# Kernel tuning notes

Measured on AMD Instinct MI355X. Metric: run time of the kernel, lower is better.

The kernel has to match this reference:

```python
import jax, jax.numpy as jnp
import numpy as np

N_NODES = 40000
N_EDGES = 640000
IN_DIM = 7
HID = 128
N_LAYERS = 5


def setup_inputs() -> dict:
    key = jax.random.key(0)
    ks = jax.random.split(key, 12)
    x = jax.random.normal(ks[0], (N_NODES, IN_DIM), dtype=jnp.float32)
    edge_index = jax.random.randint(ks[1], (2, N_EDGES), 0, N_NODES, dtype=jnp.int64)
    # shift distances away from 0 so 1/d^2 weights stay finite across 5 layers
    dist = jax.random.uniform(ks[2], (N_EDGES,), dtype=jnp.float32) + 0.5
    s_enc = 1.0 / np.sqrt(IN_DIM)
    s_hid = 1.0 / np.sqrt(HID)
    enc_W = jax.random.normal(ks[3], (HID, IN_DIM), dtype=jnp.float32) * s_enc
    enc_b = jax.random.normal(ks[4], (HID,), dtype=jnp.float32) * 0.01
    conv_W = jax.random.normal(ks[5], (N_LAYERS, HID, HID), dtype=jnp.float32) * s_hid * 0.2
    conv_b = jax.random.normal(ks[6], (N_LAYERS, HID), dtype=jnp.float32) * 0.01
    cluster_W = jax.random.normal(ks[7], (3, HID), dtype=jnp.float32) * s_hid
    cluster_b = jax.random.normal(ks[8], (3,), dtype=jnp.float32) * 0.01
    energy_W = jax.random.normal(ks[9], (1, HID), dtype=jnp.float32) * s_hid
    energy_b = jax.random.normal(ks[10], (1,), dtype=jnp.float32) * 0.01
    return {"x": x, "edge_index": edge_index, "dist": dist,
            "enc_W": enc_W, "enc_b": enc_b,
            "conv_W": conv_W, "conv_b": conv_b,
            "cluster_W": cluster_W, "cluster_b": cluster_b,
            "energy_W": energy_W, "energy_b": energy_b}


def reference(x, edge_index, dist, enc_W, enc_b, conv_W, conv_b,
              cluster_W, cluster_b, energy_W, energy_b):
    n = x.shape[0]
    src = edge_index[0]  # x_j: source nodes (PyG source_to_target flow)
    dst = edge_index[1]  # aggregation target
    w = 1.0 / jnp.square(dist + 1e-6)  # [E]
    h = x @ enc_W.T + enc_b  # [N, H]
    for l in range(conv_W.shape[0]):
        # gather -> linear -> inverse-square weight -> scatter-add
        msg = (h[src] @ conv_W[l].T + conv_b[l]) * w[:, None]  # [E, H]
        h = jax.nn.relu(jax.ops.segment_sum(msg, dst, num_segments=n))
    cluster_probs = jax.nn.softmax(h @ cluster_W.T + cluster_b, axis=-1)  # [N, 3]
    energy = h.mean(axis=0, keepdims=True) @ energy_W.T + energy_b  # [1, 1]
    stable = energy < -1.0
    return cluster_probs, energy, stable
```

## Files before the change

kernel.cpp:

```cpp
#include <hip/hip_runtime.h>
#include <hip/hip_fp16.h>

#define NN 40000
#define NE 640000
#define HID 128
#define NL 5
#define NBLK 157

typedef __attribute__((ext_vector_type(8))) short bf16x8;
typedef __attribute__((ext_vector_type(4))) float f32x4;

static __device__ __forceinline__ unsigned short f32_to_bf16_rne(float f) {
  unsigned int u = __float_as_uint(f);
  unsigned int lsb = (u >> 16) & 1u;
  u += 0x7fffu + lsb;
  return (unsigned short)(u >> 16);
}
static __device__ __forceinline__ float bf16_to_f32(unsigned short s) {
  return __uint_as_float(((unsigned int)s) << 16);
}

__global__ void encoder_wconv_kernel(const float* __restrict__ x, const float* __restrict__ encW,
                                     const float* __restrict__ encb, __half* __restrict__ h,
                                     const float* __restrict__ convW,
                                     unsigned short* __restrict__ whi,
                                     unsigned short* __restrict__ wlo) {
  int b = blockIdx.x;
  if (b < 20000) {
    int gid = b * 256 + threadIdx.x;
    int n = gid >> 7, k = gid & 127;
    const float* xp = x + n * 7;
    const float* wp = encW + k * 7;
    float acc = encb[k];
#pragma unroll
    for (int i = 0; i < 7; ++i) acc += xp[i] * wp[i];
    h[gid] = __float2half(acc);
  } else {
    int i = (b - 20000) * 256 + threadIdx.x;
    if (i < NL * HID * HID) {
      float w = convW[i];
      unsigned short hi = f32_to_bf16_rne(w);
      unsigned short lo = f32_to_bf16_rne(w - bf16_to_f32(hi));
      whi[i] = hi;
      wlo[i] = lo;
    }
  }
}

__global__ void hist_kernel(const int* __restrict__ dst, int* __restrict__ cnt,
                            int* __restrict__ rank) {
  int e = blockIdx.x * blockDim.x + threadIdx.x;
  if (e < NE) rank[e] = atomicAdd(&cnt[dst[e]], 1);
}

__global__ void partial_kernel(const int* __restrict__ cnt, int* __restrict__ blocksum) {
  __shared__ int red[4];
  int t = threadIdx.x;
  int idx = blockIdx.x * 256 + t;
  int v = idx < NN ? cnt[idx] : 0;
#pragma unroll
  for (int off = 32; off > 0; off >>= 1) v += __shfl_xor(v, off, 64);
  if ((t & 63) == 0) red[t >> 6] = v;
  __syncthreads();
  if (t == 0) blocksum[blockIdx.x] = red[0] + red[1] + red[2] + red[3];
}

__global__ void scan_small_kernel(const int* __restrict__ blocksum, int* __restrict__ blockoff,
                                  int* __restrict__ row_ptr) {
  __shared__ int sh[256];
  int t = threadIdx.x;
  int v = t < NBLK ? blocksum[t] : 0;
  sh[t] = v;
  __syncthreads();
  for (int off = 1; off < 256; off <<= 1) {
    int u = (t >= off) ? sh[t - off] : 0;
    __syncthreads();
    sh[t] += u;
    __syncthreads();
  }
  if (t < NBLK) blockoff[t] = sh[t] - v;
  if (t == 255) row_ptr[NN] = sh[255];
}

__global__ void rowptr_kernel(const int* __restrict__ cnt, const int* __restrict__ blockoff,
                              int* __restrict__ row_ptr) {
  __shared__ int sh[256];
  int t = threadIdx.x;
  int idx = blockIdx.x * 256 + t;
  int v = idx < NN ? cnt[idx] : 0;
  sh[t] = v;
  __syncthreads();
  for (int off = 1; off < 256; off <<= 1) {
    int u = (t >= off) ? sh[t - off] : 0;
    __syncthreads();
    sh[t] += u;
    __syncthreads();
  }
  if (idx < NN) row_ptr[idx] = blockoff[blockIdx.x] + sh[t] - v;
}

__global__ void scatter_kernel(const int* __restrict__ src, const int* __restrict__ dst,
                               const float* __restrict__ dist,
                               const int* __restrict__ row_ptr, const int* __restrict__ rank,
                               int2* __restrict__ csr_ew) {
  int e = blockIdx.x * blockDim.x + threadIdx.x;
  if (e >= NE) return;
  int pos = row_ptr[dst[e]] + rank[e];
  float dd = dist[e] + 1e-6f;
  float w = 1.0f / (dd * dd);
  csr_ew[pos] = make_int2(src[e], (int)__float_as_uint(w));
}

__global__ void wsum_kernel(const int* __restrict__ row_ptr, const int2* __restrict__ csr_ew,
                            float* __restrict__ wsum) {
  int n = blockIdx.x * blockDim.x + threadIdx.x;
  if (n >= NN) return;
  int s = row_ptr[n], e = row_ptr[n + 1];
  float acc = 0.f;
  for (int i = s; i < e; ++i) acc += __uint_as_float((unsigned)csr_ew[i].y);
  wsum[n] = acc;
}

__global__ void aggregate_kernel(const __half* __restrict__ h, const int* __restrict__ row_ptr,
                                 const int2* __restrict__ csr_ew,
                                 unsigned short* __restrict__ aggh,
                                 unsigned short* __restrict__ aggl) {
  int wid = (blockIdx.x * blockDim.x + threadIdx.x) >> 6;
  int lane = threadIdx.x & 63;
  if (wid >= NN) return;
  int s = __builtin_amdgcn_readfirstlane(row_ptr[wid]);
  int e = __builtin_amdgcn_readfirstlane(row_ptr[wid + 1]);
  const __half* hp = h + lane * 2;
  float ax = 0.f, ay = 0.f;
  int i = s;
  for (; i + 16 <= e; i += 16) {
    unsigned hv[16];
    float wv[16];
#pragma unroll
    for (int u = 0; u < 16; ++u) {
      int2 p = csr_ew[i + u];
      wv[u] = __uint_as_float((unsigned)p.y);
      hv[u] = *reinterpret_cast<const unsigned*>(hp + p.x * HID);
    }
#pragma unroll
    for (int u = 0; u < 16; ++u) {
      float2 f = __half22float2(*reinterpret_cast<__half2*>(&hv[u]));
      ax += wv[u] * f.x;
      ay += wv[u] * f.y;
    }
  }
  for (; i < e; ++i) {
    int2 p = csr_ew[i];
    float w = __uint_as_float((unsigned)p.y);
    float2 f = __half22float2(*reinterpret_cast<const __half2*>(hp + p.x * HID));
    ax += w * f.x;
    ay += w * f.y;
  }
  unsigned short hx = f32_to_bf16_rne(ax);
  unsigned short lx = f32_to_bf16_rne(ax - bf16_to_f32(hx));
  unsigned short hy = f32_to_bf16_rne(ay);
  unsigned short ly = f32_to_bf16_rne(ay - bf16_to_f32(hy));
  ushort2 hv2 = {hx, hy}, lv2 = {lx, ly};
  *reinterpret_cast<ushort2*>(aggh + wid * HID + lane * 2) = hv2;
  *reinterpret_cast<ushort2*>(aggl + wid * HID + lane * 2) = lv2;
}

__global__ void __launch_bounds__(256) mfma_linear_kernel(
    const unsigned short* __restrict__ aggh, const unsigned short* __restrict__ aggl,
    const unsigned short* __restrict__ whi, const unsigned short* __restrict__ wlo,
    const float* __restrict__ wsum, const float* __restrict__ b, __half* __restrict__ h) {
  int wave = threadIdx.x >> 6;
  int lane = threadIdx.x & 63;
  int node0 = blockIdx.x * 64 + wave * 16;
  int mrow = lane & 15;
  int kc = (lane >> 4) * 8;

  const unsigned short* pah = aggh + (node0 + mrow) * HID;
  const unsigned short* pal = aggl + (node0 + mrow) * HID;

  f32x4 acc[8];
#pragma unroll
  for (int t = 0; t < 8; ++t) acc[t] = (f32x4){0.f, 0.f, 0.f, 0.f};

#pragma unroll
  for (int s = 0; s < 4; ++s) {
    int joff = s * 32 + kc;
    bf16x8 ah = *reinterpret_cast<const bf16x8*>(pah + joff);
    bf16x8 al = *reinterpret_cast<const bf16x8*>(pal + joff);
#pragma unroll
    for (int t = 0; t < 8; ++t) {
      bf16x8 bh = *reinterpret_cast<const bf16x8*>(whi + (t * 16 + mrow) * HID + joff);
      bf16x8 bl = *reinterpret_cast<const bf16x8*>(wlo + (t * 16 + mrow) * HID + joff);
      acc[t] = __builtin_amdgcn_mfma_f32_16x16x32_bf16(ah, bh, acc[t], 0, 0, 0);
      acc[t] = __builtin_amdgcn_mfma_f32_16x16x32_bf16(ah, bl, acc[t], 0, 0, 0);
      acc[t] = __builtin_amdgcn_mfma_f32_16x16x32_bf16(al, bh, acc[t], 0, 0, 0);
    }
  }

  int nodeBase = node0 + (lane >> 4) * 4;
  float ws4[4];
#pragma unroll
  for (int r = 0; r < 4; ++r) ws4[r] = wsum[nodeBase + r];
#pragma unroll
  for (int t = 0; t < 8; ++t) {
    int kout = t * 16 + mrow;
    float bk = b[kout];
#pragma unroll
    for (int r = 0; r < 4; ++r) {
      float v = acc[t][r] + bk * ws4[r];
      h[(nodeBase + r) * HID + kout] = __float2half(fmaxf(v, 0.f));
    }
  }
}

__global__ void cluster_kernel(const __half* __restrict__ h, const float* __restrict__ cW,
                               const float* __restrict__ cb, float* __restrict__ out) {
  int wid = (blockIdx.x * blockDim.x + threadIdx.x) >> 6;
  int lane = threadIdx.x & 63;
  if (wid >= NN) return;
  float h0 = __half2float(h[wid * HID + lane]);
  float h1 = __half2float(h[wid * HID + 64 + lane]);
  float logit[3];
#pragma unroll
  for (int c = 0; c < 3; ++c) {
    float p = h0 * cW[c * HID + lane] + h1 * cW[c * HID + 64 + lane];
#pragma unroll
    for (int off = 32; off > 0; off >>= 1) p += __shfl_xor(p, off, 64);
    logit[c] = p + cb[c];
  }
  if (lane == 0) {
    float m = fmaxf(logit[0], fmaxf(logit[1], logit[2]));
    float e0 = expf(logit[0] - m), e1 = expf(logit[1] - m), e2 = expf(logit[2] - m);
    float inv = 1.0f / (e0 + e1 + e2);
    out[wid * 3 + 0] = e0 * inv;
    out[wid * 3 + 1] = e1 * inv;
    out[wid * 3 + 2] = e2 * inv;
  }
}

__global__ void colsum_part_kernel(const __half* __restrict__ h, float* __restrict__ partial) {
  int t = threadIdx.x;
  int col = t & 127;
  int lane_id = blockIdx.x * 2 + (t >> 7);
  float acc = 0.f;
  for (int r = lane_id; r < NN; r += 2048) acc += __half2float(h[r * HID + col]);
  partial[lane_id * HID + col] = acc;
}

__global__ void energy_final_kernel(const float* __restrict__ partial,
                                    const float* __restrict__ eW, const float* __restrict__ eb,
                                    float* __restrict__ out) {
  __shared__ float sh[8][HID];
  __shared__ float red[2];
  int t = threadIdx.x;
  int col = t & 127;
  int slot = t >> 7;
  float acc = 0.f;
  for (int i = 0; i < 256; ++i) acc += partial[(slot + 8 * i) * HID + col];
  sh[slot][col] = acc;
  __syncthreads();
  if (t < 128) {
    float s = 0.f;
#pragma unroll
    for (int j = 0; j < 8; ++j) s += sh[j][t];
    float v = s * (1.0f / NN) * eW[t];
#pragma unroll
    for (int off = 32; off > 0; off >>= 1) v += __shfl_xor(v, off, 64);
    if ((t & 63) == 0) red[t >> 6] = v;
  }
  __syncthreads();
  if (t == 0) {
    float e = red[0] + red[1] + eb[0];
    out[NN * 3] = e;
    out[NN * 3 + 1] = (e < -1.0f) ? 1.0f : 0.0f;
  }
}

extern "C" void kernel_launch(void* const* d_in, const int* in_sizes, int n_in,
                              void* d_out, int out_size, void* d_ws, size_t ws_size,
                              hipStream_t stream) {
  const float* x    = (const float*)d_in[0];
  const int*   ei   = (const int*)d_in[1];
  const float* dist = (const float*)d_in[2];
  const float* encW = (const float*)d_in[3];
  const float* encb = (const float*)d_in[4];
  const float* convW = (const float*)d_in[5];
  const float* convb = (const float*)d_in[6];
  const float* cW   = (const float*)d_in[7];
  const float* cb   = (const float*)d_in[8];
  const float* eW   = (const float*)d_in[9];
  const float* eb   = (const float*)d_in[10];
  float* out = (float*)d_out;

  char* ws = (char*)d_ws;
  __half*         h       = (__half*)        (ws + 0);
  unsigned short* aggh    = (unsigned short*)(ws + 10240000);
  unsigned short* aggl    = (unsigned short*)(ws + 20480000);
  int2*           csr_ew  = (int2*)          (ws + 30720000);
  int*            row_ptr = (int*)           (ws + 35840000);
  int*            cnt     = (int*)           (ws + 36000064);
  float*          wsum    = (float*)         (ws + 36160064);
  unsigned short* whi5    = (unsigned short*)(ws + 36320064);
  unsigned short* wlo5    = (unsigned short*)(ws + 36483904);
  int*            rank    = (int*)           (ws + 36647744);
  if (ws_size < (size_t)39207744) return;

  int*   blocksum = (int*)aggh;
  int*   blockoff = (int*)aggh + 512;
  float* partial  = (float*)aggh;

  const int* srcI = ei;
  const int* dstI = ei + NE;

  hipMemsetAsync(cnt, 0, 160000, stream);

  encoder_wconv_kernel<<<20320, 256, 0, stream>>>(x, encW, encb, h, convW, whi5, wlo5);

  hist_kernel<<<(NE + 255) / 256, 256, 0, stream>>>(dstI, cnt, rank);
  partial_kernel<<<NBLK, 256, 0, stream>>>(cnt, blocksum);
  scan_small_kernel<<<1, 256, 0, stream>>>(blocksum, blockoff, row_ptr);
  rowptr_kernel<<<NBLK, 256, 0, stream>>>(cnt, blockoff, row_ptr);
  scatter_kernel<<<(NE + 255) / 256, 256, 0, stream>>>(srcI, dstI, dist, row_ptr, rank, csr_ew);
  wsum_kernel<<<(NN + 255) / 256, 256, 0, stream>>>(row_ptr, csr_ew, wsum);

  for (int l = 0; l < NL; ++l) {
    aggregate_kernel<<<(NN * 64 + 255) / 256, 256, 0, stream>>>(h, row_ptr, csr_ew, aggh, aggl);
    mfma_linear_kernel<<<NN / 64, 256, 0, stream>>>(aggh, aggl,
                                                    whi5 + (size_t)l * HID * HID,
                                                    wlo5 + (size_t)l * HID * HID,
                                                    wsum, convb + (size_t)l * HID, h);
  }

  cluster_kernel<<<(NN * 64 + 255) / 256, 256, 0, stream>>>(h, cW, cb, out);
  colsum_part_kernel<<<1024, 256, 0, stream>>>(h, partial);
  energy_final_kernel<<<1, 1024, 0, stream>>>(partial, eW, eb, out);
}
```

Measured before the change: 410.1 us.

## Fuse neighbor aggregation into MFMA linear kernel via LDS staging

```diff
diff --git a/kernel.cpp b/kernel.cpp
--- a/kernel.cpp
+++ b/kernel.cpp
@@ -6,6 +6,7 @@
 #define HID 128
 #define NL 5
 #define NBLK 157
+#define LSTRIDE 136
 
 typedef __attribute__((ext_vector_type(8))) short bf16x8;
 typedef __attribute__((ext_vector_type(4))) float f32x4;
@@ -121,63 +122,58 @@
   wsum[n] = acc;
 }
 
-__global__ void aggregate_kernel(const __half* __restrict__ h, const int* __restrict__ row_ptr,
-                                 const int2* __restrict__ csr_ew,
-                                 unsigned short* __restrict__ aggh,
-                                 unsigned short* __restrict__ aggl) {
-  int wid = (blockIdx.x * blockDim.x + threadIdx.x) >> 6;
-  int lane = threadIdx.x & 63;
-  if (wid >= NN) return;
-  int s = __builtin_amdgcn_readfirstlane(row_ptr[wid]);
-  int e = __builtin_amdgcn_readfirstlane(row_ptr[wid + 1]);
-  const __half* hp = h + lane * 2;
-  float ax = 0.f, ay = 0.f;
-  int i = s;
-  for (; i + 16 <= e; i += 16) {
-    unsigned hv[16];
-    float wv[16];
-#pragma unroll
-    for (int u = 0; u < 16; ++u) {
-      int2 p = csr_ew[i + u];
-      wv[u] = __uint_as_float((unsigned)p.y);
-      hv[u] = *reinterpret_cast<const unsigned*>(hp + p.x * HID);
-    }
-#pragma unroll
-    for (int u = 0; u < 16; ++u) {
-      float2 f = __half22float2(*reinterpret_cast<__half2*>(&hv[u]));
-      ax += wv[u] * f.x;
-      ay += wv[u] * f.y;
-    }
-  }
-  for (; i < e; ++i) {
-    int2 p = csr_ew[i];
-    float w = __uint_as_float((unsigned)p.y);
-    float2 f = __half22float2(*reinterpret_cast<const __half2*>(hp + p.x * HID));
-    ax += w * f.x;
-    ay += w * f.y;
-  }
-  unsigned short hx = f32_to_bf16_rne(ax);
-  unsigned short lx = f32_to_bf16_rne(ax - bf16_to_f32(hx));
-  unsigned short hy = f32_to_bf16_rne(ay);
-  unsigned short ly = f32_to_bf16_rne(ay - bf16_to_f32(hy));
-  ushort2 hv2 = {hx, hy}, lv2 = {lx, ly};
-  *reinterpret_cast<ushort2*>(aggh + wid * HID + lane * 2) = hv2;
-  *reinterpret_cast<ushort2*>(aggl + wid * HID + lane * 2) = lv2;
-}
-
-__global__ void __launch_bounds__(256) mfma_linear_kernel(
-    const unsigned short* __restrict__ aggh, const unsigned short* __restrict__ aggl,
+__global__ void __launch_bounds__(256) fused_layer_kernel(
+    const __half* __restrict__ hin, const int* __restrict__ row_ptr,
+    const int2* __restrict__ csr_ew,
     const unsigned short* __restrict__ whi, const unsigned short* __restrict__ wlo,
-    const float* __restrict__ wsum, const float* __restrict__ b, __half* __restrict__ h) {
+    const float* __restrict__ wsum, const float* __restrict__ b,
+    __half* __restrict__ hout) {
+  __shared__ __align__(16) unsigned short sAh[4][16][LSTRIDE];
+  __shared__ __align__(16) unsigned short sAl[4][16][LSTRIDE];
   int wave = threadIdx.x >> 6;
   int lane = threadIdx.x & 63;
   int node0 = blockIdx.x * 64 + wave * 16;
+
+  const __half* hp = hin + lane * 2;
+  for (int t = 0; t < 16; ++t) {
+    int node = node0 + t;
+    int s = __builtin_amdgcn_readfirstlane(row_ptr[node]);
+    int e = __builtin_amdgcn_readfirstlane(row_ptr[node + 1]);
+    float ax = 0.f, ay = 0.f;
+    int i = s;
+    for (; i + 16 <= e; i += 16) {
+      unsigned hv[16];
+      float wv[16];
+#pragma unroll
+      for (int u = 0; u < 16; ++u) {
+        int2 p = csr_ew[i + u];
+        wv[u] = __uint_as_float((unsigned)p.y);
+        hv[u] = *reinterpret_cast<const unsigned*>(hp + p.x * HID);
+      }
+#pragma unroll
+      for (int u = 0; u < 16; ++u) {
+        float2 f = __half22float2(*reinterpret_cast<__half2*>(&hv[u]));
+        ax += wv[u] * f.x;
+        ay += wv[u] * f.y;
+      }
+    }
+    for (; i < e; ++i) {
+      int2 p = csr_ew[i];
+      float w = __uint_as_float((unsigned)p.y);
+      float2 f = __half22float2(*reinterpret_cast<const __half2*>(hp + p.x * HID));
+      ax += w * f.x;
+      ay += w * f.y;
+    }
+    unsigned short hx = f32_to_bf16_rne(ax), lx = f32_to_bf16_rne(ax - bf16_to_f32(hx));
+    unsigned short hy = f32_to_bf16_rne(ay), ly = f32_to_bf16_rne(ay - bf16_to_f32(hy));
+    ushort2 hv2 = {hx, hy}, lv2 = {lx, ly};
+    *reinterpret_cast<ushort2*>(&sAh[wave][t][lane * 2]) = hv2;
+    *reinterpret_cast<ushort2*>(&sAl[wave][t][lane * 2]) = lv2;
+  }
+
   int mrow = lane & 15;
   int kc = (lane >> 4) * 8;
 
-  const unsigned short* pah = aggh + (node0 + mrow) * HID;
-  const unsigned short* pal = aggl + (node0 + mrow) * HID;
-
   f32x4 acc[8];
 #pragma unroll
   for (int t = 0; t < 8; ++t) acc[t] = (f32x4){0.f, 0.f, 0.f, 0.f};
@@ -185,8 +181,8 @@
 #pragma unroll
   for (int s = 0; s < 4; ++s) {
     int joff = s * 32 + kc;
-    bf16x8 ah = *reinterpret_cast<const bf16x8*>(pah + joff);
-    bf16x8 al = *reinterpret_cast<const bf16x8*>(pal + joff);
+    bf16x8 ah = *reinterpret_cast<const bf16x8*>(&sAh[wave][mrow][joff]);
+    bf16x8 al = *reinterpret_cast<const bf16x8*>(&sAl[wave][mrow][joff]);
 #pragma unroll
     for (int t = 0; t < 8; ++t) {
       bf16x8 bh = *reinterpret_cast<const bf16x8*>(whi + (t * 16 + mrow) * HID + joff);
@@ -208,7 +204,7 @@
 #pragma unroll
     for (int r = 0; r < 4; ++r) {
       float v = acc[t][r] + bk * ws4[r];
-      h[(nodeBase + r) * HID + kout] = __float2half(fmaxf(v, 0.f));
+      hout[(nodeBase + r) * HID + kout] = __float2half(fmaxf(v, 0.f));
     }
   }
 }
@@ -293,9 +289,9 @@
   float* out = (float*)d_out;
 
   char* ws = (char*)d_ws;
-  __half*         h       = (__half*)        (ws + 0);
-  unsigned short* aggh    = (unsigned short*)(ws + 10240000);
-  unsigned short* aggl    = (unsigned short*)(ws + 20480000);
+  __half*         h1      = (__half*)        (ws + 0);
+  __half*         h2      = (__half*)        (ws + 10240000);
+  char*           scratch = (char*)          (ws + 20480000);
   int2*           csr_ew  = (int2*)          (ws + 30720000);
   int*            row_ptr = (int*)           (ws + 35840000);
   int*            cnt     = (int*)           (ws + 36000064);
@@ -305,16 +301,16 @@
   int*            rank    = (int*)           (ws + 36647744);
   if (ws_size < (size_t)39207744) return;
 
-  int*   blocksum = (int*)aggh;
-  int*   blockoff = (int*)aggh + 512;
-  float* partial  = (float*)aggh;
+  int*   blocksum = (int*)scratch;
+  int*   blockoff = (int*)scratch + 512;
+  float* partial  = (float*)scratch;
 
   const int* srcI = ei;
   const int* dstI = ei + NE;
 
   hipMemsetAsync(cnt, 0, 160000, stream);
 
-  encoder_wconv_kernel<<<20320, 256, 0, stream>>>(x, encW, encb, h, convW, whi5, wlo5);
+  encoder_wconv_kernel<<<20320, 256, 0, stream>>>(x, encW, encb, h1, convW, whi5, wlo5);
 
   hist_kernel<<<(NE + 255) / 256, 256, 0, stream>>>(dstI, cnt, rank);
   partial_kernel<<<NBLK, 256, 0, stream>>>(cnt, blocksum);
@@ -323,15 +319,17 @@
   scatter_kernel<<<(NE + 255) / 256, 256, 0, stream>>>(srcI, dstI, dist, row_ptr, rank, csr_ew);
   wsum_kernel<<<(NN + 255) / 256, 256, 0, stream>>>(row_ptr, csr_ew, wsum);
 
+  __half* hin = h1;
+  __half* hout = h2;
   for (int l = 0; l < NL; ++l) {
-    aggregate_kernel<<<(NN * 64 + 255) / 256, 256, 0, stream>>>(h, row_ptr, csr_ew, aggh, aggl);
-    mfma_linear_kernel<<<NN / 64, 256, 0, stream>>>(aggh, aggl,
+    fused_layer_kernel<<<NN / 64, 256, 0, stream>>>(hin, row_ptr, csr_ew,
                                                     whi5 + (size_t)l * HID * HID,
                                                     wlo5 + (size_t)l * HID * HID,
-                                                    wsum, convb + (size_t)l * HID, h);
-  }
-
-  cluster_kernel<<<(NN * 64 + 255) / 256, 256, 0, stream>>>(h, cW, cb, out);
-  colsum_part_kernel<<<1024, 256, 0, stream>>>(h, partial);
+                                                    wsum, convb + (size_t)l * HID, hout);
+    __half* tmp = hin; hin = hout; hout = tmp;
+  }
+
+  cluster_kernel<<<(NN * 64 + 255) / 256, 256, 0, stream>>>(hin, cW, cb, out);
+  colsum_part_kernel<<<1024, 256, 0, stream>>>(hin, partial);
   energy_final_kernel<<<1, 1024, 0, stream>>>(partial, eW, eb, out);
 }
```

After: 493.8 us. +20.4%, slower.
